# Kernel tuning notes

Hardware: AMD Instinct MI355X
Metric: run time of the kernel (lower is better)

The kernel has to match this reference:

```python
import math
import jax, jax.numpy as jnp
import numpy as np

B, L, U, D, H, VOCAB = 8, 512, 24, 1024, 16, 54945
T = 3 * U
CSK = 1024
BN_EPS = 1e-5


def _heads(x, H):
    b, t, dm = x.shape
    d = dm // H
    return x.reshape(b, t, H, d).transpose(0, 2, 1, 3)  # [B,H,T,d]


def _masked_attn(x, mask, edge_type, Wq, bq, Wk, bk, Wv, bv, rel_table, n_heads):
    # Faithful to MaskedSelfAttention.forward with edge_type: at query row i the
    # query/key layers have accumulated sum_{j<=i} rel_layer_j added (in-place += in torch).
    b, t, dm = x.shape
    d = dm // n_heads
    Q = _heads(x @ Wq + bq, n_heads)
    K = _heads(x @ Wk + bk, n_heads)
    V = _heads(x @ Wv + bv, n_heads)
    # rel_table[edge_type]: [B, i(rel row), p(pos), D] -> [B, i, H, p, d]
    R = rel_table[edge_type].reshape(b, t, t, n_heads, d).transpose(0, 1, 3, 2, 4)
    S = jnp.cumsum(R, axis=1)  # inclusive prefix sum over relation-row index i
    # S_diag[b,h,i,d] = S[b,i,h,i,d] : accumulated rel at query position i
    S_diag = jnp.moveaxis(jnp.diagonal(S, axis1=1, axis2=3), -1, 2)  # [B,H,T,d]
    A = Q + S_diag  # effective query rows
    # scores[b,h,i,k] = A[b,h,i] . (K[b,h,k] + S[b,i,h,k])
    scores = (jnp.einsum('bhid,bhkd->bhik', A, K)
              + jnp.einsum('bhid,bihkd->bhik', A, S)) / math.sqrt(d)
    scores = jnp.where(mask[:, None, :, :] == 0, -1e9, scores)
    probs = jax.nn.softmax(scores, axis=-1)  # dropout omitted (eval mode)
    ctx = jnp.einsum('bhik,bhkd->bhid', probs, V)
    return ctx.transpose(0, 2, 1, 3).reshape(b, t, dm)


def setup_inputs() -> dict:
    key = jax.random.key(0)
    ks = jax.random.split(key, 30)
    p = lambda k, shape: (jax.random.normal(k, shape, jnp.float32) * 0.02)
    rel_table = p(ks[8], (8, D)).at[0].set(0.0)  # padding_idx=0
    inp = {
        'hidden_states': jax.random.normal(ks[0], (B, L, D), jnp.float32),
        'emo_csk': jax.random.normal(ks[1], (B, U, CSK), jnp.float32),
        'Wq': p(ks[2], (D, D)), 'bq': jnp.zeros((D,), jnp.float32),
        'Wk': p(ks[3], (D, D)), 'bk': jnp.zeros((D,), jnp.float32),
        'Wv': p(ks[4], (D, D)), 'bv': jnp.zeros((D,), jnp.float32),
        'rel_table': rel_table,
        'fusion_W': p(ks[5], (2 * D, D)), 'fusion_b': jnp.zeros((D,), jnp.float32),
        'bn_gamma': jnp.ones((CSK,), jnp.float32), 'bn_beta': jnp.zeros((CSK,), jnp.float32),
        'bn_mean': p(ks[6], (CSK,)), 'bn_var': jnp.ones((CSK,), jnp.float32),
        'csk_W': p(ks[7], (CSK, D)), 'csk_b': jnp.zeros((D,), jnp.float32),
        'emo_W': p(ks[9], (D, 6)), 'emo_b': jnp.zeros((6,), jnp.float32),
        'str_W': p(ks[10], (D, 8)), 'str_b': jnp.zeros((8,), jnp.float32),
        'bow_W': p(ks[11], (D, VOCAB)),
        'trans_cls_index': jnp.sort(jax.random.randint(ks[12], (B, U), 2, L), axis=-1),
        'trans_graph': jax.random.randint(ks[13], (B, T, T), 0, 2, jnp.int32),
        'inter_graph': jax.random.randint(ks[14], (B, T, T), 0, 2, jnp.int32),
        'trans_edge_type': jax.random.randint(ks[15], (B, T, T), 0, 8, jnp.int32),
        'inter_edge_type': jax.random.randint(ks[16], (B, T, T), 0, 8, jnp.int32),
    }
    return inp


def reference(hidden_states, emo_csk, Wq, bq, Wk, bk, Wv, bv, rel_table,
              fusion_W, fusion_b, bn_gamma, bn_beta, bn_mean, bn_var,
              csk_W, csk_b, emo_W, emo_b, str_W, str_b, bow_W,
              trans_cls_index, trans_graph, inter_graph,
              trans_edge_type, inter_edge_type):
    b, l, dm = hidden_states.shape
    u = trans_cls_index.shape[1]
    # per-conversation CLS gather (all indices valid: text_len == U)
    cls_emb = jnp.take_along_axis(hidden_states, trans_cls_index[:, :, None], axis=1)  # [B,U,D]
    sem_cls_embs = cls_emb
    # BatchNorm1d (eval: running stats) + linear 1024->D
    csk_norm = (emo_csk - bn_mean) / jnp.sqrt(bn_var + BN_EPS) * bn_gamma + bn_beta
    csk_proj = csk_norm @ csk_W + csk_b  # [B,U,D]
    # _prepare_for_transition: [cls, cls, cls(+csk if not last)] per utterance -> T=3U
    trans_in = jnp.repeat(cls_emb, 3, axis=1)  # [B,3U,D]
    not_last = (jnp.arange(u) < u - 1).astype(csk_proj.dtype)[None, :, None]
    trans_in = trans_in.at[:, 2::3, :].add(csk_proj * not_last)
    attn = lambda x, m, e: _masked_attn(x, m, e, Wq, bq, Wk, bk, Wv, bv, rel_table, H)
    trans_out = attn(trans_in, trans_graph, trans_edge_type)
    inter_out = attn(trans_out, inter_graph, inter_edge_type)
    gate = jax.nn.sigmoid(jnp.concatenate([trans_out, inter_out], axis=-1) @ fusion_W + fusion_b)
    outputs = (1.0 - gate) * inter_out + gate * trans_out
    sem_trans = outputs[:, 0::3]
    stra_trans = outputs[:, 1::3]
    emo_trans = outputs[:, 2::3]
    last_stra_state = stra_trans[:, u - 1]
    delta = sem_trans - sem_cls_embs
    last_delta = delta[:, u - 1]
    bow_logits = delta @ bow_W
    emotion_logits = emo_trans @ emo_W + emo_b
    strategy_logits = stra_trans @ str_W + str_b
    return (last_stra_state, emo_trans, last_delta, sem_cls_embs,
            strategy_logits, emotion_logits, bow_logits)
```

## Files before the change

kernel.cpp:

```cpp
#include <hip/hip_runtime.h>
#include <math.h>

#define BB 8
#define LL 512
#define UU 24
#define DD 1024
#define HH 16
#define DH 64
#define TT 72
#define CSKN 1024
#define NVOCAB 54945

typedef __attribute__((ext_vector_type(8))) short bf16x8;
typedef __attribute__((ext_vector_type(4))) float f32x4;

__device__ inline unsigned short f2b(float x) {
    unsigned u = __float_as_uint(x);
    unsigned r = u + 0x7FFFu + ((u >> 16) & 1u);
    return (unsigned short)(r >> 16);
}
__device__ inline unsigned pack2(float lo, float hi) {
    return (unsigned)f2b(lo) | ((unsigned)f2b(hi) << 16);
}
__device__ inline void dec8(uint2 c, float* cr) {
    cr[0] = (float)( c.x        & 0xff); cr[1] = (float)((c.x >>  8) & 0xff);
    cr[2] = (float)((c.x >> 16) & 0xff); cr[3] = (float)((c.x >> 24) & 0xff);
    cr[4] = (float)( c.y        & 0xff); cr[5] = (float)((c.y >>  8) & 0xff);
    cr[6] = (float)((c.y >> 16) & 0xff); cr[7] = (float)((c.y >> 24) & 0xff);
}

__global__ __launch_bounds__(256) void k_gather_bn(const float* __restrict__ hidden,
        const int* __restrict__ idx, float* __restrict__ sem_cls, float* __restrict__ trans_in,
        const float* __restrict__ x, const float* __restrict__ g,
        const float* __restrict__ be, const float* __restrict__ mu,
        const float* __restrict__ var, float* __restrict__ y)
{
    int bid = blockIdx.x;
    if (bid < BB*UU) {
        int b = bid / UU, u = bid % UU;
        int row = idx[b*UU + u];
        const float* src = hidden + ((size_t)(b*LL + row))*DD;
        float* d0 = trans_in + ((size_t)(b*TT + 3*u))*DD;
        float* sc = sem_cls + ((size_t)(b*UU + u))*DD;
        for (int d = threadIdx.x; d < DD; d += 256) {
            float v = src[d];
            sc[d] = v;
            d0[d] = v; d0[DD + d] = v; d0[2*DD + d] = v;
        }
    } else {
        int i = (bid - BB*UU)*256 + threadIdx.x;
        int n = BB*UU*CSKN;
        if (i < n) {
            int c = i % CSKN;
            y[i] = (x[i] - mu[c]) * (1.0f/sqrtf(var[c] + 1e-5f)) * g[c] + be[c];
        }
    }
}

template<int EPI>
__global__ __launch_bounds__(256) void mm64(
        const float* __restrict__ A1, const float* __restrict__ A2, int K1,
        const float* __restrict__ Bm, const float* __restrict__ bias,
        const float* __restrict__ ep1, const float* __restrict__ ep2,
        float* __restrict__ C, int N, int K)
{
    __shared__ __align__(16) unsigned short As[2][64][72];
    __shared__ __align__(16) unsigned short Bs[2][64][72];
    int tid = threadIdx.x;
    int wave = tid >> 6, lane = tid & 63;
    int l16 = lane & 15, g = lane >> 4;
    int wm = wave & 1, wn = wave >> 1;
    int row0 = blockIdx.y * 64, col0 = blockIdx.x * 64;

    int ar = tid >> 2, akq = (tid & 3) * 16;
    int bj0 = (tid & 31) * 2, kp = tid >> 5;
    float4 a0, a1, a2, a3;
    float2 b0[4], b1[4];

    auto loadT = [&](int k0) {
        int kk = k0 + akq;
        const float* src = (kk < K1) ? A1 + (size_t)(row0+ar)*K1 + kk
                                     : A2 + (size_t)(row0+ar)*(K-K1) + (kk-K1);
        a0 = *(const float4*)src;      a1 = *(const float4*)(src+4);
        a2 = *(const float4*)(src+8);  a3 = *(const float4*)(src+12);
        #pragma unroll
        for (int s = 0; s < 4; ++s) {
            int kb = 2*(kp + 8*s);
            const float* bp = Bm + (size_t)(k0 + kb)*N + col0 + bj0;
            b0[s] = *(const float2*)bp;
            b1[s] = *(const float2*)(bp + N);
        }
    };
    auto storeT = [&](int buf) {
        unsigned* da = (unsigned*)&As[buf][ar][akq];
        da[0]=pack2(a0.x,a0.y); da[1]=pack2(a0.z,a0.w);
        da[2]=pack2(a1.x,a1.y); da[3]=pack2(a1.z,a1.w);
        da[4]=pack2(a2.x,a2.y); da[5]=pack2(a2.z,a2.w);
        da[6]=pack2(a3.x,a3.y); da[7]=pack2(a3.z,a3.w);
        #pragma unroll
        for (int s = 0; s < 4; ++s) {
            int kb = 2*(kp + 8*s);
            *(unsigned*)&Bs[buf][bj0  ][kb] = pack2(b0[s].x, b1[s].x);
            *(unsigned*)&Bs[buf][bj0+1][kb] = pack2(b0[s].y, b1[s].y);
        }
    };

    f32x4 acc[2][2] = {};
    loadT(0); storeT(0);
    __syncthreads();
    int nt = K / 64;
    for (int t = 0; t < nt; ++t) {
        int cur = t & 1;
        if (t + 1 < nt) loadT((t+1)*64);
        #pragma unroll
        for (int kk = 0; kk < 2; ++kk) {
            bf16x8 af[2], bfr[2];
            #pragma unroll
            for (int mf = 0; mf < 2; ++mf) af[mf] = *(const bf16x8*)&As[cur][wm*32 + mf*16 + l16][kk*32 + g*8];
            #pragma unroll
            for (int nf = 0; nf < 2; ++nf) bfr[nf] = *(const bf16x8*)&Bs[cur][wn*32 + nf*16 + l16][kk*32 + g*8];
            #pragma unroll
            for (int mf = 0; mf < 2; ++mf)
                #pragma unroll
                for (int nf = 0; nf < 2; ++nf)
                    acc[mf][nf] = __builtin_amdgcn_mfma_f32_16x16x32_bf16(af[mf], bfr[nf], acc[mf][nf], 0, 0, 0);
        }
        if (t + 1 < nt) storeT(cur ^ 1);
        __syncthreads();
    }
    #pragma unroll
    for (int mf = 0; mf < 2; ++mf)
        #pragma unroll
        for (int nf = 0; nf < 2; ++nf) {
            int cc = col0 + wn*32 + nf*16 + l16;
            float bv = bias[cc];
            #pragma unroll
            for (int r = 0; r < 4; ++r) {
                int rr = row0 + wm*32 + mf*16 + g*4 + r;
                float v = acc[mf][nf][r] + bv;
                if (EPI == 3) {
                    float gg = 1.0f/(1.0f + __expf(-v));
                    float tv = ep1[(size_t)rr*N + cc];
                    float iv = ep2[(size_t)rr*N + cc];
                    C[(size_t)rr*N + cc] = gg*tv + (1.0f - gg)*iv;
                } else {
                    int bq = rr / UU, uq = rr % UU;
                    if (uq < UU-1) {
                        float* dst = &C[((size_t)(bq*TT + 3*uq + 2))*DD + cc];
                        *dst += v;
                    }
                }
            }
        }
}

__global__ __launch_bounds__(256) void mm_qkv(
        const float* __restrict__ x,
        const float* __restrict__ W0, const float* __restrict__ W1, const float* __restrict__ W2,
        const float* __restrict__ v0, const float* __restrict__ v1, const float* __restrict__ v2,
        float* __restrict__ C0, float* __restrict__ C1, float* __restrict__ C2)
{
    __shared__ __align__(16) unsigned short As[2][64][72];
    __shared__ __align__(16) unsigned short Bs[2][128][72];
    int which = blockIdx.x >> 3;
    int col0 = (blockIdx.x & 7) * 128;
    int row0 = blockIdx.y * 64;
    const float* W  = (which == 0) ? W0 : (which == 1) ? W1 : W2;
    const float* bb = (which == 0) ? v0 : (which == 1) ? v1 : v2;
    float*       C  = (which == 0) ? C0 : (which == 1) ? C1 : C2;
    int tid = threadIdx.x;
    int wave = tid >> 6, lane = tid & 63;
    int l16 = lane & 15, g = lane >> 4;
    int wm = wave & 1, wn = wave >> 1;

    int ar = tid >> 2, akq = (tid & 3) * 16;
    int bj0 = (tid & 63) * 2, kp = tid >> 6;
    float4 a0, a1, a2, a3;
    float2 b0[8], b1[8];

    auto loadT = [&](int k0) {
        const float* src = x + (size_t)(row0+ar)*DD + k0 + akq;
        a0 = *(const float4*)src;      a1 = *(const float4*)(src+4);
        a2 = *(const float4*)(src+8);  a3 = *(const float4*)(src+12);
        #pragma unroll
        for (int s = 0; s < 8; ++s) {
            int kb = 2*(kp + 4*s);
            const float* bp = W + (size_t)(k0 + kb)*DD + col0 + bj0;
            b0[s] = *(const float2*)bp;
            b1[s] = *(const float2*)(bp + DD);
        }
    };
    auto storeT = [&](int buf) {
        unsigned* da = (unsigned*)&As[buf][ar][akq];
        da[0]=pack2(a0.x,a0.y); da[1]=pack2(a0.z,a0.w);
        da[2]=pack2(a1.x,a1.y); da[3]=pack2(a1.z,a1.w);
        da[4]=pack2(a2.x,a2.y); da[5]=pack2(a2.z,a2.w);
        da[6]=pack2(a3.x,a3.y); da[7]=pack2(a3.z,a3.w);
        #pragma unroll
        for (int s = 0; s < 8; ++s) {
            int kb = 2*(kp + 4*s);
            *(unsigned*)&Bs[buf][bj0  ][kb] = pack2(b0[s].x, b1[s].x);
            *(unsigned*)&Bs[buf][bj0+1][kb] = pack2(b0[s].y, b1[s].y);
        }
    };

    f32x4 acc[2][4] = {};
    loadT(0); storeT(0);
    __syncthreads();
    for (int t = 0; t < 16; ++t) {
        int cur = t & 1;
        if (t < 15) loadT((t+1)*64);
        #pragma unroll
        for (int kk = 0; kk < 2; ++kk) {
            bf16x8 af[2], bfr[4];
            #pragma unroll
            for (int mf = 0; mf < 2; ++mf) af[mf] = *(const bf16x8*)&As[cur][wm*32 + mf*16 + l16][kk*32 + g*8];
            #pragma unroll
            for (int nf = 0; nf < 4; ++nf) bfr[nf] = *(const bf16x8*)&Bs[cur][wn*64 + nf*16 + l16][kk*32 + g*8];
            #pragma unroll
            for (int mf = 0; mf < 2; ++mf)
                #pragma unroll
                for (int nf = 0; nf < 4; ++nf)
                    acc[mf][nf] = __builtin_amdgcn_mfma_f32_16x16x32_bf16(af[mf], bfr[nf], acc[mf][nf], 0, 0, 0);
        }
        if (t < 15) storeT(cur ^ 1);
        __syncthreads();
    }
    #pragma unroll
    for (int mf = 0; mf < 2; ++mf)
        #pragma unroll
        for (int nf = 0; nf < 4; ++nf) {
            int cc = col0 + wn*64 + nf*16 + l16;
            float bv = bb[cc];
            #pragma unroll
            for (int r = 0; r < 4; ++r) {
                int rr = row0 + wm*32 + mf*16 + g*4 + r;
                C[(size_t)rr*DD + cc] = acc[mf][nf][r] + bv;
            }
        }
}

__global__ __launch_bounds__(256, 1) void mm_bow(
        const unsigned short* __restrict__ Ab, const float* __restrict__ Bm,
        float* __restrict__ C)
{
    __shared__ __align__(16) unsigned short A_lds[192][136];
    const int N = NVOCAB;
    int tid = threadIdx.x;
    int lane = tid & 63, wave = tid >> 6;
    int l16 = lane & 15, g = lane >> 4;
    int col = blockIdx.x * 64 + wave * 16 + l16;
    int colc = (col < N) ? col : (N - 1);
    const float* bbase = Bm + (size_t)(g * 8) * N + colc;

    int4 areg0, areg1, areg2, areg3, areg4, areg5, areg6, areg7, areg8, areg9, areg10, areg11;
#define AIDX(i) int r##i = ((i)*256 + tid) >> 4, c##i = (((i)*256 + tid) & 15) * 8
    AIDX(0); AIDX(1); AIDX(2); AIDX(3); AIDX(4); AIDX(5);
    AIDX(6); AIDX(7); AIDX(8); AIDX(9); AIDX(10); AIDX(11);
#undef AIDX
#define LOADA(s) {                                                             \
        const unsigned short* ab = Ab + (s)*128;                               \
        areg0  = *(const int4*)(ab + (size_t)r0*DD  + c0);                     \
        areg1  = *(const int4*)(ab + (size_t)r1*DD  + c1);                     \
        areg2  = *(const int4*)(ab + (size_t)r2*DD  + c2);                     \
        areg3  = *(const int4*)(ab + (size_t)r3*DD  + c3);                     \
        areg4  = *(const int4*)(ab + (size_t)r4*DD  + c4);                     \
        areg5  = *(const int4*)(ab + (size_t)r5*DD  + c5);                     \
        areg6  = *(const int4*)(ab + (size_t)r6*DD  + c6);                     \
        areg7  = *(const int4*)(ab + (size_t)r7*DD  + c7);                     \
        areg8  = *(const int4*)(ab + (size_t)r8*DD  + c8);                     \
        areg9  = *(const int4*)(ab + (size_t)r9*DD  + c9);                     \
        areg10 = *(const int4*)(ab + (size_t)r10*DD + c10);                    \
        areg11 = *(const int4*)(ab + (size_t)r11*DD + c11);                    \
    }
#define WRITEA() {                                                             \
        *(int4*)&A_lds[r0][c0]   = areg0;  *(int4*)&A_lds[r1][c1]   = areg1;   \
        *(int4*)&A_lds[r2][c2]   = areg2;  *(int4*)&A_lds[r3][c3]   = areg3;   \
        *(int4*)&A_lds[r4][c4]   = areg4;  *(int4*)&A_lds[r5][c5]   = areg5;   \
        *(int4*)&A_lds[r6][c6]   = areg6;  *(int4*)&A_lds[r7][c7]   = areg7;   \
        *(int4*)&A_lds[r8][c8]   = areg8;  *(int4*)&A_lds[r9][c9]   = areg9;   \
        *(int4*)&A_lds[r10][c10] = areg10; *(int4*)&A_lds[r11][c11] = areg11;  \
    }

    f32x4 acc[12] = {};
    float bs[4][8];

#define LOADB(dst, t_) { const float* bp = bbase + (size_t)(t_) * 32 * N;      \
        _Pragma("unroll") for (int j = 0; j < 8; ++j) dst[j] = bp[(size_t)j * N]; }
#define PACKB(fr, sv) { _Pragma("unroll") for (int j = 0; j < 8; ++j)          \
        ((unsigned short*)&fr)[j] = f2b(sv[j]); }

    LOADA(0); WRITEA();
    #pragma unroll
    for (int p = 0; p < 4; ++p) LOADB(bs[p], p);
    __syncthreads();

    for (int s = 0; s < 8; ++s) {
        if (s < 7) LOADA(s + 1);
        #pragma unroll
        for (int p = 0; p < 4; ++p) {
            int P = s*4 + p;
            bf16x8 fr;
            PACKB(fr, bs[p]);
            if (P + 4 < 32) LOADB(bs[p], P + 4);
            #pragma unroll
            for (int mf = 0; mf < 12; ++mf) {
                bf16x8 af = *(const bf16x8*)&A_lds[mf*16 + l16][p*32 + g*8];
                acc[mf] = __builtin_amdgcn_mfma_f32_16x16x32_bf16(af, fr, acc[mf], 0, 0, 0);
            }
        }
        if (s < 7) {
            __syncthreads();
            WRITEA();
            __syncthreads();
        }
    }
#undef LOADA
#undef WRITEA
#undef LOADB
#undef PACKB
    if (col < N) {
        #pragma unroll
        for (int mf = 0; mf < 12; ++mf)
            #pragma unroll
            for (int r = 0; r < 4; ++r)
                C[(size_t)(mf * 16 + g * 4 + r) * N + col] = acc[mf][r];
    }
}

__global__ __launch_bounds__(512) void k_attn(const float* __restrict__ Qb,
        const float* __restrict__ Kg, const float* __restrict__ Vg,
        const int* __restrict__ et, const float* __restrict__ rel,
        const int* __restrict__ mask, float* __restrict__ out)
{
    int bid = blockIdx.x;
    int is = bid & 1;
    int h  = (bid >> 1) & (HH-1);
    int b  = bid >> 5;
    int lo = is * (TT/2);
    __shared__ float K_sh[DH][TT+1];
    __shared__ float V_sh[TT][DH];
    __shared__ uint2 cnt_sh[TT/2][TT];
    __shared__ __align__(16) unsigned char un_raw[6400];
    float (*rel_sh)[DH] = (float(*)[DH])un_raw;
    float (*a_row)[DH]  = (float(*)[DH])(un_raw + 2048);
    float (*p_row)[TT]  = (float(*)[TT])(un_raw + 4096);
    unsigned char* e_sh = un_raw;
    int tid = threadIdx.x;
    int lane = tid & 63, w = tid >> 6;

    for (int idx = tid; idx < TT*16; idx += 512) {
        int r = idx >> 4, q4 = (idx & 15) * 4;
        size_t goff = ((size_t)(b*TT + r))*DD + h*DH + q4;
        float4 kv = *(const float4*)&Kg[goff];
        K_sh[q4  ][r] = kv.x; K_sh[q4+1][r] = kv.y;
        K_sh[q4+2][r] = kv.z; K_sh[q4+3][r] = kv.w;
        float4 vv = *(const float4*)&Vg[goff];
        *(float4*)&V_sh[r][q4] = vv;
    }
    for (int idx = tid; idx < (TT*TT)/4; idx += 512) {
        int4 v = ((const int4*)(et + (size_t)b*TT*TT))[idx];
        unsigned pk = (unsigned)v.x | ((unsigned)v.y << 8) | ((unsigned)v.z << 16) | ((unsigned)v.w << 24);
        *(unsigned*)&e_sh[idx*4] = pk;
    }
    __syncthreads();
    if (tid < TT) {
        unsigned lo32 = 0, hi32 = 0;
        int iend = lo + TT/2;
        for (int i = 0; i < iend; ++i) {
            int r = e_sh[i*TT + tid];
            if (r < 4) lo32 += 1u << (8*r); else hi32 += 1u << (8*(r-4));
            if (i >= lo) cnt_sh[i - lo][tid] = make_uint2(lo32, hi32);
        }
    }
    __syncthreads();
    if (tid < 128) {
        int r = tid >> 4, q4 = (tid & 15) * 4;
        *(float4*)&rel_sh[r][q4] = *(const float4*)&rel[r*DD + h*DH + q4];
    }
    __syncthreads();

    auto processRow = [&](float q, int ii) {
        int i = lo + ii;
        size_t rowoff = (size_t)(b*TT + i);
        float crd[8]; dec8(cnt_sh[ii][i], crd);
        float a = q;
        #pragma unroll
        for (int r = 0; r < 8; ++r) a += crd[r]*rel_sh[r][lane];
        a_row[w][lane] = a;
        float arr[8];
        #pragma unroll
        for (int r = 0; r < 8; ++r) {
            float pr = a * rel_sh[r][lane];
            #pragma unroll
            for (int off = 32; off; off >>= 1) pr += __shfl_xor(pr, off);
            arr[r] = pr;
        }
        float s1;
        {
            int t = lane;
            float s = 0.0f;
            #pragma unroll
            for (int d0 = 0; d0 < DH; d0 += 4) {
                float4 av = *(const float4*)&a_row[w][d0];
                s += av.x*K_sh[d0][t] + av.y*K_sh[d0+1][t]
                   + av.z*K_sh[d0+2][t] + av.w*K_sh[d0+3][t];
            }
            float cr2[8]; dec8(cnt_sh[ii][t], cr2);
            float s2v = cr2[0]*arr[0] + cr2[1]*arr[1] + cr2[2]*arr[2] + cr2[3]*arr[3]
                      + cr2[4]*arr[4] + cr2[5]*arr[5] + cr2[6]*arr[6] + cr2[7]*arr[7];
            int m = mask[rowoff*TT + t];
            s1 = (m == 0) ? -1e9f : (s + s2v)*0.125f;
        }
        float s2 = -1e30f;
        if (lane < TT - DH) {
            int t = DH + lane;
            float s = 0.0f;
            #pragma unroll
            for (int d0 = 0; d0 < DH; d0 += 4) {
                float4 av = *(const float4*)&a_row[w][d0];
                s += av.x*K_sh[d0][t] + av.y*K_sh[d0+1][t]
                   + av.z*K_sh[d0+2][t] + av.w*K_sh[d0+3][t];
            }
            float cr2[8]; dec8(cnt_sh[ii][t], cr2);
            float s2v = cr2[0]*arr[0] + cr2[1]*arr[1] + cr2[2]*arr[2] + cr2[3]*arr[3]
                      + cr2[4]*arr[4] + cr2[5]*arr[5] + cr2[6]*arr[6] + cr2[7]*arr[7];
            int m = mask[rowoff*TT + t];
            s2 = (m == 0) ? -1e9f : (s + s2v)*0.125f;
        }
        float mx = fmaxf(s1, s2);
        #pragma unroll
        for (int off = 32; off; off >>= 1) mx = fmaxf(mx, __shfl_xor(mx, off));
        float e1 = __expf(s1 - mx);
        float e2 = (lane < TT - DH) ? __expf(s2 - mx) : 0.0f;
        float sm = e1 + e2;
        #pragma unroll
        for (int off = 32; off; off >>= 1) sm += __shfl_xor(sm, off);
        float inv = 1.0f / sm;
        p_row[w][lane] = e1 * inv;
        if (lane < TT - DH) p_row[w][DH + lane] = e2 * inv;
        float o = 0.0f;
        #pragma unroll 8
        for (int t = 0; t < TT; ++t) o += p_row[w][t] * V_sh[t][lane];
        out[rowoff*DD + h*DH + lane] = o;
    };

    float qv0, qv1, qv2, qv3, qv4 = 0.0f;
    {
        size_t base = ((size_t)(b*TT + lo + w))*DD + h*DH + lane;
        qv0 = Qb[base];
        qv1 = Qb[base + (size_t)8*DD];
        qv2 = Qb[base + (size_t)16*DD];
        qv3 = Qb[base + (size_t)24*DD];
        if (w < 4) qv4 = Qb[base + (size_t)32*DD];
    }
    processRow(qv0, w);
    processRow(qv1, w + 8);
    processRow(qv2, w + 16);
    processRow(qv3, w + 24);
    if (w < 4) processRow(qv4, w + 32);
}

__global__ __launch_bounds__(256) void k_finlog(const float* __restrict__ outs,
        const float* __restrict__ sem_cls,
        const float* __restrict__ strW, const float* __restrict__ strB,
        const float* __restrict__ emoW, const float* __restrict__ emoB,
        float* __restrict__ o_last_stra, float* __restrict__ o_emo,
        float* __restrict__ o_last_delta, float* __restrict__ o_str,
        float* __restrict__ o_emo_log, unsigned short* __restrict__ deltaB)
{
    __shared__ float part[14][16];
    int bid = blockIdx.x; int b = bid / UU, u = bid % UU;
    const float* sem = outs + ((size_t)(b*TT + 3*u))*DD;
    const float* st  = sem + DD;
    const float* em  = st + DD;
    const float* sc  = sem_cls + ((size_t)(b*UU + u))*DD;
    unsigned short* de = deltaB + ((size_t)(b*UU + u))*DD;
    float* oe = o_emo + ((size_t)(b*UU + u))*DD;
    int t = threadIdx.x;
    for (int d = t; d < DD; d += 256) {
        float dl = sem[d] - sc[d];
        de[d] = f2b(dl); oe[d] = em[d];
        if (u == UU-1) { o_last_stra[b*DD + d] = st[d]; o_last_delta[b*DD + d] = dl; }
    }
    if (t < 224) {
        int o = t >> 4, c = t & 15;
        float s = 0.0f;
        if (o < 8) {
            for (int d = c*64; d < c*64 + 64; ++d) s += st[d]*strW[d*8 + o];
        } else {
            int j = o - 8;
            for (int d = c*64; d < c*64 + 64; ++d) s += em[d]*emoW[d*6 + j];
        }
        part[o][c] = s;
    }
    __syncthreads();
    if (t < 14) {
        float s = 0.0f;
        #pragma unroll
        for (int c2 = 0; c2 < 16; ++c2) s += part[t][c2];
        if (t < 8) o_str[(b*UU + u)*8 + t] = s + strB[t];
        else       o_emo_log[(b*UU + u)*6 + (t-8)] = s + emoB[t-8];
    }
}

extern "C" void kernel_launch(void* const* d_in, const int* in_sizes, int n_in,
                              void* d_out, int out_size, void* d_ws, size_t ws_size,
                              hipStream_t stream)
{
    const float* hidden  = (const float*)d_in[0];
    const float* emo_csk = (const float*)d_in[1];
    const float* Wq  = (const float*)d_in[2];
    const float* bq  = (const float*)d_in[3];
    const float* Wk  = (const float*)d_in[4];
    const float* bk  = (const float*)d_in[5];
    const float* Wv  = (const float*)d_in[6];
    const float* bv  = (const float*)d_in[7];
    const float* rel = (const float*)d_in[8];
    const float* fusW = (const float*)d_in[9];
    const float* fusB = (const float*)d_in[10];
    const float* bng = (const float*)d_in[11];
    const float* bnb = (const float*)d_in[12];
    const float* bnm = (const float*)d_in[13];
    const float* bnv = (const float*)d_in[14];
    const float* cskW = (const float*)d_in[15];
    const float* cskB = (const float*)d_in[16];
    const float* emoW = (const float*)d_in[17];
    const float* emoB = (const float*)d_in[18];
    const float* strW = (const float*)d_in[19];
    const float* strB = (const float*)d_in[20];
    const float* bowW = (const float*)d_in[21];
    const int* clsIdx = (const int*)d_in[22];
    const int* tGraph = (const int*)d_in[23];
    const int* iGraph = (const int*)d_in[24];
    const int* tEdge  = (const int*)d_in[25];
    const int* iEdge  = (const int*)d_in[26];

    float* out = (float*)d_out;
    float* o_last_stra  = out;
    float* o_emo_trans  = out + 8192;
    float* o_last_delta = out + 204800;
    float* o_sem_cls    = out + 212992;
    float* o_str_log    = out + 409600;
    float* o_emo_log    = out + 411136;
    float* o_bow        = out + 412288;

    float* ws = (float*)d_ws;
    const int SZ_BTD = BB*TT*DD;
    const int SZ_BUD = BB*UU*DD;
    float* trans_in  = ws;
    float* Qb        = trans_in + SZ_BTD;
    float* Kb        = Qb + SZ_BTD;
    float* Vb        = Kb + SZ_BTD;
    float* trans_out = Vb + SZ_BTD;
    float* inter_out = trans_out + SZ_BTD;
    float* outsB     = inter_out + SZ_BTD;
    float* csk_norm  = outsB + SZ_BTD;
    unsigned short* deltaB = (unsigned short*)(csk_norm + SZ_BUD);

    k_gather_bn<<<dim3(BB*UU + (BB*UU*CSKN+255)/256), dim3(256), 0, stream>>>(
            hidden, clsIdx, o_sem_cls, trans_in, emo_csk, bng, bnb, bnm, bnv, csk_norm);
    mm64<4><<<dim3(16, 3), dim3(256), 0, stream>>>(csk_norm, nullptr, CSKN, cskW, cskB,
            nullptr, nullptr, trans_in, DD, CSKN);

    auto attention = [&](const float* x, const int* graph, const int* edge, float* ctx_out) {
        mm_qkv<<<dim3(24, (BB*TT)/64), dim3(256), 0, stream>>>(x, Wq, Wk, Wv, bq, bk, bv, Qb, Kb, Vb);
        k_attn<<<dim3(BB*HH*2), dim3(512), 0, stream>>>(Qb, Kb, Vb, edge, rel, graph, ctx_out);
    };
    attention(trans_in, tGraph, tEdge, trans_out);
    attention(trans_out, iGraph, iEdge, inter_out);

    mm64<3><<<dim3(16, (BB*TT)/64), dim3(256), 0, stream>>>(trans_out, inter_out, DD, fusW, fusB,
            trans_out, inter_out, outsB, DD, 2*DD);

    k_finlog<<<dim3(BB*UU), dim3(256), 0, stream>>>(outsB, o_sem_cls, strW, strB, emoW, emoB,
            o_last_stra, o_emo_trans, o_last_delta, o_str_log, o_emo_log, deltaB);

    mm_bow<<<dim3((NVOCAB+63)/64), dim3(256), 0, stream>>>(deltaB, bowW, o_bow);
}
```

Measured before the change: 275.3 us.

## Fuse output slicing into fusion GEMM epilogue and shrink QKV tile

The fusion-gate GEMM epilogue now also writes the per-utterance outputs directly: the bf16 delta for the bow GEMM, the emotion states, and the last strategy and delta rows. This strips the copy and delta work out of the finlog kernel, which becomes a small logits-only kernel. Separately, the QKV GEMM tile width drops from 128 to 64 columns, doubling the grid to 48x9 blocks. The smaller tile gives more blocks on the many CUs in exchange for less reuse of the A tile.

```diff
diff --git a/kernel.cpp b/kernel.cpp
--- a/kernel.cpp
+++ b/kernel.cpp
@@ -62,7 +62,10 @@
         const float* __restrict__ A1, const float* __restrict__ A2, int K1,
         const float* __restrict__ Bm, const float* __restrict__ bias,
         const float* __restrict__ ep1, const float* __restrict__ ep2,
-        float* __restrict__ C, int N, int K)
+        float* __restrict__ C, int N, int K,
+        const float* __restrict__ sem_cls, unsigned short* __restrict__ deltaB,
+        float* __restrict__ o_emo, float* __restrict__ o_lstra,
+        float* __restrict__ o_ldelta)
 {
     __shared__ __align__(16) unsigned short As[2][64][72];
     __shared__ __align__(16) unsigned short Bs[2][64][72];
@@ -138,17 +141,29 @@
             for (int r = 0; r < 4; ++r) {
                 int rr = row0 + wm*32 + mf*16 + g*4 + r;
                 float v = acc[mf][nf][r] + bv;
-                if (EPI == 3) {
-                    float gg = 1.0f/(1.0f + __expf(-v));
-                    float tv = ep1[(size_t)rr*N + cc];
-                    float iv = ep2[(size_t)rr*N + cc];
-                    C[(size_t)rr*N + cc] = gg*tv + (1.0f - gg)*iv;
-                } else {
+                if (EPI == 4) {
                     int bq = rr / UU, uq = rr % UU;
                     if (uq < UU-1) {
                         float* dst = &C[((size_t)(bq*TT + 3*uq + 2))*DD + cc];
                         *dst += v;
                     }
+                } else {
+                    float gg = 1.0f/(1.0f + __expf(-v));
+                    float tv = ep1[(size_t)rr*N + cc];
+                    float iv = ep2[(size_t)rr*N + cc];
+                    float bl = gg*tv + (1.0f - gg)*iv;
+                    C[(size_t)rr*N + cc] = bl;
+                    int b = rr / TT, tt = rr % TT;
+                    int m3 = tt % 3, u = tt / 3;
+                    if (m3 == 0) {
+                        float dl = bl - sem_cls[((size_t)(b*UU + u))*DD + cc];
+                        deltaB[((size_t)(b*UU + u))*DD + cc] = f2b(dl);
+                        if (u == UU-1) o_ldelta[b*DD + cc] = dl;
+                    } else if (m3 == 1) {
+                        if (u == UU-1) o_lstra[b*DD + cc] = bl;
+                    } else {
+                        o_emo[((size_t)(b*UU + u))*DD + cc] = bl;
+                    }
                 }
             }
         }
@@ -161,9 +176,9 @@
         float* __restrict__ C0, float* __restrict__ C1, float* __restrict__ C2)
 {
     __shared__ __align__(16) unsigned short As[2][64][72];
-    __shared__ __align__(16) unsigned short Bs[2][128][72];
-    int which = blockIdx.x >> 3;
-    int col0 = (blockIdx.x & 7) * 128;
+    __shared__ __align__(16) unsigned short Bs[2][64][72];
+    int which = blockIdx.x >> 4;
+    int col0 = (blockIdx.x & 15) * 64;
     int row0 = blockIdx.y * 64;
     const float* W  = (which == 0) ? W0 : (which == 1) ? W1 : W2;
     const float* bb = (which == 0) ? v0 : (which == 1) ? v1 : v2;
@@ -174,17 +189,17 @@
     int wm = wave & 1, wn = wave >> 1;
 
     int ar = tid >> 2, akq = (tid & 3) * 16;
-    int bj0 = (tid & 63) * 2, kp = tid >> 6;
+    int bj0 = (tid & 31) * 2, kp = tid >> 5;
     float4 a0, a1, a2, a3;
-    float2 b0[8], b1[8];
+    float2 b0[4], b1[4];
 
     auto loadT = [&](int k0) {
         const float* src = x + (size_t)(row0+ar)*DD + k0 + akq;
         a0 = *(const float4*)src;      a1 = *(const float4*)(src+4);
         a2 = *(const float4*)(src+8);  a3 = *(const float4*)(src+12);
         #pragma unroll
-        for (int s = 0; s < 8; ++s) {
-            int kb = 2*(kp + 4*s);
+        for (int s = 0; s < 4; ++s) {
+            int kb = 2*(kp + 8*s);
             const float* bp = W + (size_t)(k0 + kb)*DD + col0 + bj0;
             b0[s] = *(const float2*)bp;
             b1[s] = *(const float2*)(bp + DD);
@@ -197,14 +212,14 @@
         da[4]=pack2(a2.x,a2.y); da[5]=pack2(a2.z,a2.w);
         da[6]=pack2(a3.x,a3.y); da[7]=pack2(a3.z,a3.w);
         #pragma unroll
-        for (int s = 0; s < 8; ++s) {
-            int kb = 2*(kp + 4*s);
+        for (int s = 0; s < 4; ++s) {
+            int kb = 2*(kp + 8*s);
             *(unsigned*)&Bs[buf][bj0  ][kb] = pack2(b0[s].x, b1[s].x);
             *(unsigned*)&Bs[buf][bj0+1][kb] = pack2(b0[s].y, b1[s].y);
         }
     };
 
-    f32x4 acc[2][4] = {};
+    f32x4 acc[2][2] = {};
     loadT(0); storeT(0);
     __syncthreads();
     for (int t = 0; t < 16; ++t) {
@@ -212,15 +227,15 @@
         if (t < 15) loadT((t+1)*64);
         #pragma unroll
         for (int kk = 0; kk < 2; ++kk) {
-            bf16x8 af[2], bfr[4];
+            bf16x8 af[2], bfr[2];
             #pragma unroll
             for (int mf = 0; mf < 2; ++mf) af[mf] = *(const bf16x8*)&As[cur][wm*32 + mf*16 + l16][kk*32 + g*8];
             #pragma unroll
-            for (int nf = 0; nf < 4; ++nf) bfr[nf] = *(const bf16x8*)&Bs[cur][wn*64 + nf*16 + l16][kk*32 + g*8];
+            for (int nf = 0; nf < 2; ++nf) bfr[nf] = *(const bf16x8*)&Bs[cur][wn*32 + nf*16 + l16][kk*32 + g*8];
             #pragma unroll
             for (int mf = 0; mf < 2; ++mf)
                 #pragma unroll
-                for (int nf = 0; nf < 4; ++nf)
+                for (int nf = 0; nf < 2; ++nf)
                     acc[mf][nf] = __builtin_amdgcn_mfma_f32_16x16x32_bf16(af[mf], bfr[nf], acc[mf][nf], 0, 0, 0);
         }
         if (t < 15) storeT(cur ^ 1);
@@ -229,8 +244,8 @@
     #pragma unroll
     for (int mf = 0; mf < 2; ++mf)
         #pragma unroll
-        for (int nf = 0; nf < 4; ++nf) {
-            int cc = col0 + wn*64 + nf*16 + l16;
+        for (int nf = 0; nf < 2; ++nf) {
+            int cc = col0 + wn*32 + nf*16 + l16;
             float bv = bb[cc];
             #pragma unroll
             for (int r = 0; r < 4; ++r) {
@@ -461,28 +476,16 @@
     if (w < 4) processRow(qv4, w + 32);
 }
 
-__global__ __launch_bounds__(256) void k_finlog(const float* __restrict__ outs,
-        const float* __restrict__ sem_cls,
+__global__ __launch_bounds__(256) void k_logits(const float* __restrict__ outs,
         const float* __restrict__ strW, const float* __restrict__ strB,
         const float* __restrict__ emoW, const float* __restrict__ emoB,
-        float* __restrict__ o_last_stra, float* __restrict__ o_emo,
-        float* __restrict__ o_last_delta, float* __restrict__ o_str,
-        float* __restrict__ o_emo_log, unsigned short* __restrict__ deltaB)
+        float* __restrict__ o_str, float* __restrict__ o_emo_log)
 {
     __shared__ float part[14][16];
     int bid = blockIdx.x; int b = bid / UU, u = bid % UU;
-    const float* sem = outs + ((size_t)(b*TT + 3*u))*DD;
-    const float* st  = sem + DD;
-    const float* em  = st + DD;
-    const float* sc  = sem_cls + ((size_t)(b*UU + u))*DD;
-    unsigned short* de = deltaB + ((size_t)(b*UU + u))*DD;
-    float* oe = o_emo + ((size_t)(b*UU + u))*DD;
+    const float* st = outs + ((size_t)(b*TT + 3*u + 1))*DD;
+    const float* em = st + DD;
     int t = threadIdx.x;
-    for (int d = t; d < DD; d += 256) {
-        float dl = sem[d] - sc[d];
-        de[d] = f2b(dl); oe[d] = em[d];
-        if (u == UU-1) { o_last_stra[b*DD + d] = st[d]; o_last_delta[b*DD + d] = dl; }
-    }
     if (t < 224) {
         int o = t >> 4, c = t & 15;
         float s = 0.0f;
@@ -561,20 +564,21 @@
     k_gather_bn<<<dim3(BB*UU + (BB*UU*CSKN+255)/256), dim3(256), 0, stream>>>(
             hidden, clsIdx, o_sem_cls, trans_in, emo_csk, bng, bnb, bnm, bnv, csk_norm);
     mm64<4><<<dim3(16, 3), dim3(256), 0, stream>>>(csk_norm, nullptr, CSKN, cskW, cskB,
-            nullptr, nullptr, trans_in, DD, CSKN);
+            nullptr, nullptr, trans_in, DD, CSKN, nullptr, nullptr, nullptr, nullptr, nullptr);
 
     auto attention = [&](const float* x, const int* graph, const int* edge, float* ctx_out) {
-        mm_qkv<<<dim3(24, (BB*TT)/64), dim3(256), 0, stream>>>(x, Wq, Wk, Wv, bq, bk, bv, Qb, Kb, Vb);
+        mm_qkv<<<dim3(48, (BB*TT)/64), dim3(256), 0, stream>>>(x, Wq, Wk, Wv, bq, bk, bv, Qb, Kb, Vb);
         k_attn<<<dim3(BB*HH*2), dim3(512), 0, stream>>>(Qb, Kb, Vb, edge, rel, graph, ctx_out);
     };
     attention(trans_in, tGraph, tEdge, trans_out);
     attention(trans_out, iGraph, iEdge, inter_out);
 
-    mm64<3><<<dim3(16, (BB*TT)/64), dim3(256), 0, stream>>>(trans_out, inter_out, DD, fusW, fusB,
-            trans_out, inter_out, outsB, DD, 2*DD);
-
-    k_finlog<<<dim3(BB*UU), dim3(256), 0, stream>>>(outsB, o_sem_cls, strW, strB, emoW, emoB,
-            o_last_stra, o_emo_trans, o_last_delta, o_str_log, o_emo_log, deltaB);
+    mm64<5><<<dim3(16, (BB*TT)/64), dim3(256), 0, stream>>>(trans_out, inter_out, DD, fusW, fusB,
+            trans_out, inter_out, outsB, DD, 2*DD,
+            o_sem_cls, deltaB, o_emo_trans, o_last_stra, o_last_delta);
+
+    k_logits<<<dim3(BB*UU), dim3(256), 0, stream>>>(outsB, strW, strB, emoW, emoB,
+            o_str_log, o_emo_log);
 
     mm_bow<<<dim3((NVOCAB+63)/64), dim3(256), 0, stream>>>(deltaB, bowW, o_bow);
 }
```

Measured after the change: 263.9 us (median of 3 runs). -4.2%, faster.
